# Kernel optimization log

Hardware: AMD Instinct MI355X
Metric: run time of the kernel (lower is better)

The kernel has to match this reference:

```python
import jax, jax.numpy as jnp
import numpy as np

N = 100000   # full-order dimension (mesh nodes)
n = 10       # reduced basis size
M_CLUSTERS = 8
K = 16       # neighbors per node
B = 4        # batch
MU = 20.0


def setup_inputs() -> dict:
    key = jax.random.key(0)
    k1, k2, k3, k4, k5, k6, k7 = jax.random.split(key, 7)
    x = jax.random.normal(k1, (B, N), dtype=jnp.float32)
    # torch.nn.Linear default init scale ~ 1/sqrt(fan_in)
    W_enc = jax.random.normal(k2, (n, N), dtype=jnp.float32) / np.sqrt(N)
    W_dec = jax.random.normal(k3, (n, N), dtype=jnp.float32) / np.sqrt(N)
    W_bw = jax.random.normal(k4, (n * M_CLUSTERS, n), dtype=jnp.float32) / np.sqrt(n)
    # small neighbor distances so every bubble window has a positive entry
    neighbour_distance = jax.random.uniform(k5, (N, K), dtype=jnp.float32) * 0.05
    neighbour_id = jax.random.randint(k6, (N, K), 0, N)
    clustering_labels = jax.random.randint(k7, (N,), 0, M_CLUSTERS)
    return {"x": x, "W_enc": W_enc, "W_dec": W_dec, "W_bw": W_bw,
            "neighbour_distance": neighbour_distance,
            "neighbour_id": neighbour_id,
            "clustering_labels": clustering_labels}


def reference(x, W_enc, W_dec, W_bw, neighbour_distance, neighbour_id, clustering_labels):
    # encode: Linear(N, n, bias=False)
    enc = x @ W_enc.T                                   # [B, n]
    # bandwidths: sigmoid + affine into [4/(60*mu), 1/60]
    bw = jax.nn.sigmoid(enc @ W_bw.T)                   # [B, n*m]
    lo = 4.0 / 60.0 / MU
    bw = (1.0 / 60.0 - lo) * bw + lo
    bw = bw.reshape(-1, n, M_CLUSTERS)                  # [B, n, m]
    bw = bw[:, :, clustering_labels]                    # [B, n, N] per-node bandwidth
    # bubble window over neighbors (vectorized over all groups at once;
    # group loop in the original writes disjoint node slices -> identical math)
    d2 = neighbour_distance ** 2                        # [N, K]
    denom = (bw * MU) ** 2                              # [B, n, N]
    window = jax.nn.relu(1.0 - d2[None, None] / denom[..., None])  # [B, n, N, K]
    window = window / jnp.sum(window, axis=-1, keepdims=True)
    # gather neighbor basis values: decoder.weight[:, neighbour_id]
    basis_nb = W_dec[:, neighbour_id]                   # [n, N, K]
    smoothed = jnp.einsum('cNk,bcNk->bcN', basis_nb, window)  # [B, n, N]
    # decode: enc [B,1,n] bmm smoothed [B,n,N] -> [B,N]
    return jnp.einsum('bc,bcN->bN', enc, smoothed)
```

## Files before the change

### kernel.cpp

```cpp
#include <hip/hip_runtime.h>
#include <math.h>

#define NN 100000
#define NF 10
#define MC 8
#define KK 16
#define BB 4
#define MUF 20.0f

#define ENC_SLICES 32
#define ENC_BLOCKS (BB * NF * ENC_SLICES)
#define TR_BLOCKS  ((NN + 255) / 256)

__device__ __forceinline__ float frcp(float x) {
#if __has_builtin(__builtin_amdgcn_rcpf)
    return __builtin_amdgcn_rcpf(x);
#else
    return 1.0f / x;
#endif
}

template <bool TR>
__global__ __launch_bounds__(256) void k_prep(const float* __restrict__ x,
                                              const float* __restrict__ Wenc,
                                              const float* __restrict__ Wdec,
                                              float* __restrict__ part,
                                              float* __restrict__ Wt) {
    int blk = blockIdx.x;
    if (blk < ENC_BLOCKS) {
        int pair  = blk >> 5;
        int slice = blk & 31;
        int b = pair / NF, c = pair % NF;
        const int chunk = NN / ENC_SLICES;
        int j0 = slice * chunk;
        int j1 = j0 + chunk;
        const float* xp = x + (size_t)b * NN;
        const float* wp = Wenc + (size_t)c * NN;
        float acc = 0.f;
        for (int j = j0 + threadIdx.x; j < j1; j += 256)
            acc = fmaf(xp[j], wp[j], acc);
#pragma unroll
        for (int off = 32; off; off >>= 1) acc += __shfl_down(acc, off);
        __shared__ float red[4];
        if ((threadIdx.x & 63) == 0) red[threadIdx.x >> 6] = acc;
        __syncthreads();
        if (threadIdx.x == 0) part[blk] = red[0] + red[1] + red[2] + red[3];
    } else if (TR) {
        int j = (blk - ENC_BLOCKS) * 256 + threadIdx.x;
        if (j < NN) {
            float tmp[16];
#pragma unroll
            for (int c = 0; c < NF; ++c) tmp[c] = Wdec[(size_t)c * NN + j];
#pragma unroll
            for (int c = NF; c < 16; ++c) tmp[c] = 0.f;
            float4* o = (float4*)(Wt + (size_t)j * 16);
            o[0] = make_float4(tmp[0], tmp[1], tmp[2], tmp[3]);
            o[1] = make_float4(tmp[4], tmp[5], tmp[6], tmp[7]);
            o[2] = make_float4(tmp[8], tmp[9], tmp[10], tmp[11]);
            o[3] = make_float4(tmp[12], tmp[13], tmp[14], tmp[15]);
        }
    }
}

template <bool TR>
__global__ __launch_bounds__(256) void k_main(const float* __restrict__ ndist,
                                              const int* __restrict__ nbid,
                                              const int* __restrict__ labels,
                                              const float* __restrict__ part,
                                              const float* __restrict__ Wbw,
                                              const float* __restrict__ Wsrc,
                                              float* __restrict__ out) {
    __shared__ float s_enc[BB * NF];
    __shared__ float s_dinv[BB * NF * MC];
    int tid = threadIdx.x;
    if (tid < BB * NF) {
        const float* p = part + tid * ENC_SLICES;
        float s = 0.f;
#pragma unroll
        for (int i = 0; i < ENC_SLICES; ++i) s += p[i];
        s_enc[tid] = s;
    }
    __syncthreads();
    for (int t = tid; t < BB * NF * MC; t += 256) {
        int b = t / (NF * MC);
        int r = t % (NF * MC);
        float z = 0.f;
#pragma unroll
        for (int c = 0; c < NF; ++c) z = fmaf(s_enc[b * NF + c], Wbw[r * NF + c], z);
        float sig = 1.f / (1.f + __expf(-z));
        const float lo = (float)(4.0 / 60.0 / 20.0);
        const float sc = (float)(1.0 / 60.0 - 4.0 / 60.0 / 20.0);
        float bwv = fmaf(sc, sig, lo) * MUF;
        s_dinv[t] = frcp(bwv * bwv);
    }
    __syncthreads();

    int g = blockIdx.x * 256 + tid;
    int j = g >> 1;
    if (j >= NN) return;
    int bh = (g & 1) << 1;

    int lab = labels[j];
    float dA[NF], dB[NF];
#pragma unroll
    for (int c = 0; c < NF; ++c) {
        dA[c] = s_dinv[(bh)     * (NF * MC) + c * MC + lab];
        dB[c] = s_dinv[(bh + 1) * (NF * MC) + c * MC + lab];
    }

    const float4* dp = (const float4*)(ndist + (size_t)j * KK);
    float4 q0 = dp[0], q1 = dp[1], q2 = dp[2], q3 = dp[3];
    const int4* np = (const int4*)(nbid + (size_t)j * KK);
    int4 i0 = np[0], i1 = np[1], i2 = np[2], i3 = np[3];
    float nd[KK] = {q0.x, q0.y, q0.z, q0.w, q1.x, q1.y, q1.z, q1.w,
                    q2.x, q2.y, q2.z, q2.w, q3.x, q3.y, q3.z, q3.w};
    int nb[KK] = {i0.x, i0.y, i0.z, i0.w, i1.x, i1.y, i1.z, i1.w,
                  i2.x, i2.y, i2.z, i2.w, i3.x, i3.y, i3.z, i3.w};

    float wsA[NF], smA[NF], wsB[NF], smB[NF];
#pragma unroll
    for (int c = 0; c < NF; ++c) { wsA[c] = 0.f; smA[c] = 0.f; wsB[c] = 0.f; smB[c] = 0.f; }

#pragma unroll
    for (int k = 0; k < KK; ++k) {
        float d = nd[k];
        float dd = d * d;
        float bas[12];
        if (TR) {
            const float4* bp = (const float4*)(Wsrc + (size_t)(unsigned)nb[k] * 16);
            float4 b0 = bp[0], b1 = bp[1], b2 = bp[2];
            bas[0] = b0.x; bas[1] = b0.y; bas[2] = b0.z; bas[3] = b0.w;
            bas[4] = b1.x; bas[5] = b1.y; bas[6] = b1.z; bas[7] = b1.w;
            bas[8] = b2.x; bas[9] = b2.y; bas[10] = b2.z; bas[11] = b2.w;
        } else {
#pragma unroll
            for (int c = 0; c < NF; ++c) bas[c] = Wsrc[(size_t)c * NN + nb[k]];
        }
#pragma unroll
        for (int c = 0; c < NF; ++c) {
            float wA = fmaxf(fmaf(-dd, dA[c], 1.f), 0.f);
            wsA[c] += wA; smA[c] = fmaf(wA, bas[c], smA[c]);
            float wB = fmaxf(fmaf(-dd, dB[c], 1.f), 0.f);
            wsB[c] += wB; smB[c] = fmaf(wB, bas[c], smB[c]);
        }
    }

    float accA = 0.f, accB = 0.f;
#pragma unroll
    for (int c = 0; c < NF; ++c) {
        accA = fmaf(s_enc[bh * NF + c],       smA[c] * frcp(wsA[c]), accA);
        accB = fmaf(s_enc[(bh + 1) * NF + c], smB[c] * frcp(wsB[c]), accB);
    }
    out[(size_t)bh * NN + j]       = accA;
    out[(size_t)(bh + 1) * NN + j] = accB;
}

extern "C" void kernel_launch(void* const* d_in, const int* in_sizes, int n_in,
                              void* d_out, int out_size, void* d_ws, size_t ws_size,
                              hipStream_t stream) {
    const float* x      = (const float*)d_in[0];
    const float* Wenc   = (const float*)d_in[1];
    const float* Wdec   = (const float*)d_in[2];
    const float* Wbw    = (const float*)d_in[3];
    const float* ndist  = (const float*)d_in[4];
    const int*   nbid   = (const int*)d_in[5];
    const int*   labels = (const int*)d_in[6];
    float* out = (float*)d_out;

    float* part = (float*)d_ws;
    float* Wt   = (float*)((char*)d_ws + 8192);
    size_t need = 8192 + (size_t)NN * 16 * sizeof(float);
    bool tr = (ws_size >= need);

    int main_blocks = (NN * 2 + 255) / 256;

    if (tr) {
        k_prep<true><<<ENC_BLOCKS + TR_BLOCKS, 256, 0, stream>>>(x, Wenc, Wdec, part, Wt);
        k_main<true><<<main_blocks, 256, 0, stream>>>(ndist, nbid, labels, part, Wbw, Wt, out);
    } else {
        k_prep<false><<<ENC_BLOCKS, 256, 0, stream>>>(x, Wenc, Wdec, part, nullptr);
        k_main<false><<<main_blocks, 256, 0, stream>>>(ndist, nbid, labels, part, Wbw, Wdec, out);
    }
}
```

Before: 112.7 us.

## Fuse encoder dot products across batch and split main work by feature

The encoder stage now has each block compute all 40 batch-feature dot products over one chunk of nodes, so x and W_enc are each read once instead of once per pair. Partial sums go through a two-level reduction at the start of the main kernel. The main kernel's two threads per node now split the features (4+1 each) and cover all four batches, then combine results with a lane shuffle. Each thread gathers 5 basis values per neighbour instead of 12, which lowers gather traffic per thread. The cost is a longer reduction prologue in every main block and more per-thread register state.

New measurement: 116.0 us. +2.9%, slower.

```diff
diff --git a/kernel.cpp b/kernel.cpp
--- a/kernel.cpp
+++ b/kernel.cpp
@@ -8,9 +8,9 @@
 #define BB 4
 #define MUF 20.0f
 
-#define ENC_SLICES 32
-#define ENC_BLOCKS (BB * NF * ENC_SLICES)
-#define TR_BLOCKS  ((NN + 255) / 256)
+#define PB  200
+#define JCH (NN / PB)
+#define TRB ((NN + 255) / 256)
 
 __device__ __forceinline__ float frcp(float x) {
 #if __has_builtin(__builtin_amdgcn_rcpf)
@@ -27,26 +27,43 @@
                                               float* __restrict__ part,
                                               float* __restrict__ Wt) {
     int blk = blockIdx.x;
-    if (blk < ENC_BLOCKS) {
-        int pair  = blk >> 5;
-        int slice = blk & 31;
-        int b = pair / NF, c = pair % NF;
-        const int chunk = NN / ENC_SLICES;
-        int j0 = slice * chunk;
-        int j1 = j0 + chunk;
-        const float* xp = x + (size_t)b * NN;
-        const float* wp = Wenc + (size_t)c * NN;
-        float acc = 0.f;
-        for (int j = j0 + threadIdx.x; j < j1; j += 256)
-            acc = fmaf(xp[j], wp[j], acc);
-#pragma unroll
-        for (int off = 32; off; off >>= 1) acc += __shfl_down(acc, off);
-        __shared__ float red[4];
-        if ((threadIdx.x & 63) == 0) red[threadIdx.x >> 6] = acc;
+    if (blk < PB) {
+        int j0 = blk * JCH;
+        float acc[BB * NF];
+#pragma unroll
+        for (int i = 0; i < BB * NF; ++i) acc[i] = 0.f;
+        for (int jj = threadIdx.x; jj < JCH; jj += 256) {
+            int j = j0 + jj;
+            float xv[BB], wv[NF];
+#pragma unroll
+            for (int b = 0; b < BB; ++b) xv[b] = x[(size_t)b * NN + j];
+#pragma unroll
+            for (int c = 0; c < NF; ++c) wv[c] = Wenc[(size_t)c * NN + j];
+#pragma unroll
+            for (int b = 0; b < BB; ++b)
+#pragma unroll
+                for (int c = 0; c < NF; ++c)
+                    acc[b * NF + c] = fmaf(xv[b], wv[c], acc[b * NF + c]);
+        }
+#pragma unroll
+        for (int i = 0; i < BB * NF; ++i) {
+            float v = acc[i];
+#pragma unroll
+            for (int off = 32; off; off >>= 1) v += __shfl_down(v, off, 64);
+            acc[i] = v;
+        }
+        __shared__ float red[BB * NF][4];
+        int lane = threadIdx.x & 63, w = threadIdx.x >> 6;
+        if (lane == 0) {
+#pragma unroll
+            for (int i = 0; i < BB * NF; ++i) red[i][w] = acc[i];
+        }
         __syncthreads();
-        if (threadIdx.x == 0) part[blk] = red[0] + red[1] + red[2] + red[3];
+        if (threadIdx.x < BB * NF)
+            part[threadIdx.x * PB + blk] =
+                red[threadIdx.x][0] + red[threadIdx.x][1] + red[threadIdx.x][2] + red[threadIdx.x][3];
     } else if (TR) {
-        int j = (blk - ENC_BLOCKS) * 256 + threadIdx.x;
+        int j = (blk - PB) * 256 + threadIdx.x;
         if (j < NN) {
             float tmp[16];
 #pragma unroll
@@ -72,12 +89,21 @@
                                               float* __restrict__ out) {
     __shared__ float s_enc[BB * NF];
     __shared__ float s_dinv[BB * NF * MC];
+    __shared__ float s_red[BB * NF][6];
     int tid = threadIdx.x;
+    if (tid < 240) {
+        int p = tid / 6, s = tid % 6;
+        int i0 = s * 34, i1 = i0 + 34 > PB ? PB : i0 + 34;
+        const float* pp = part + p * PB;
+        float sum = 0.f;
+        for (int i = i0; i < i1; ++i) sum += pp[i];
+        s_red[p][s] = sum;
+    }
+    __syncthreads();
     if (tid < BB * NF) {
-        const float* p = part + tid * ENC_SLICES;
         float s = 0.f;
 #pragma unroll
-        for (int i = 0; i < ENC_SLICES; ++i) s += p[i];
+        for (int i = 0; i < 6; ++i) s += s_red[tid][i];
         s_enc[tid] = s;
     }
     __syncthreads();
@@ -98,61 +124,77 @@
     int g = blockIdx.x * 256 + tid;
     int j = g >> 1;
     if (j >= NN) return;
-    int bh = (g & 1) << 1;
+    int cg = g & 1;
+    int cbase = cg * 4;
+    int cext  = 8 + cg;
 
     int lab = labels[j];
-    float dA[NF], dB[NF];
-#pragma unroll
-    for (int c = 0; c < NF; ++c) {
-        dA[c] = s_dinv[(bh)     * (NF * MC) + c * MC + lab];
-        dB[c] = s_dinv[(bh + 1) * (NF * MC) + c * MC + lab];
+    float dv[BB][5];
+#pragma unroll
+    for (int b = 0; b < BB; ++b) {
+#pragma unroll
+        for (int i = 0; i < 4; ++i)
+            dv[b][i] = s_dinv[b * (NF * MC) + (cbase + i) * MC + lab];
+        dv[b][4] = s_dinv[b * (NF * MC) + cext * MC + lab];
     }
 
     const float4* dp = (const float4*)(ndist + (size_t)j * KK);
     float4 q0 = dp[0], q1 = dp[1], q2 = dp[2], q3 = dp[3];
     const int4* np = (const int4*)(nbid + (size_t)j * KK);
-    int4 i0 = np[0], i1 = np[1], i2 = np[2], i3 = np[3];
+    int4 i0v = np[0], i1v = np[1], i2v = np[2], i3v = np[3];
     float nd[KK] = {q0.x, q0.y, q0.z, q0.w, q1.x, q1.y, q1.z, q1.w,
                     q2.x, q2.y, q2.z, q2.w, q3.x, q3.y, q3.z, q3.w};
-    int nb[KK] = {i0.x, i0.y, i0.z, i0.w, i1.x, i1.y, i1.z, i1.w,
-                  i2.x, i2.y, i2.z, i2.w, i3.x, i3.y, i3.z, i3.w};
-
-    float wsA[NF], smA[NF], wsB[NF], smB[NF];
-#pragma unroll
-    for (int c = 0; c < NF; ++c) { wsA[c] = 0.f; smA[c] = 0.f; wsB[c] = 0.f; smB[c] = 0.f; }
+    int nb[KK] = {i0v.x, i0v.y, i0v.z, i0v.w, i1v.x, i1v.y, i1v.z, i1v.w,
+                  i2v.x, i2v.y, i2v.z, i2v.w, i3v.x, i3v.y, i3v.z, i3v.w};
+
+    float ws[BB][5], sm[BB][5];
+#pragma unroll
+    for (int b = 0; b < BB; ++b)
+#pragma unroll
+        for (int i = 0; i < 5; ++i) { ws[b][i] = 0.f; sm[b][i] = 0.f; }
 
 #pragma unroll
     for (int k = 0; k < KK; ++k) {
         float d = nd[k];
         float dd = d * d;
-        float bas[12];
+        float bas[5];
         if (TR) {
-            const float4* bp = (const float4*)(Wsrc + (size_t)(unsigned)nb[k] * 16);
-            float4 b0 = bp[0], b1 = bp[1], b2 = bp[2];
-            bas[0] = b0.x; bas[1] = b0.y; bas[2] = b0.z; bas[3] = b0.w;
-            bas[4] = b1.x; bas[5] = b1.y; bas[6] = b1.z; bas[7] = b1.w;
-            bas[8] = b2.x; bas[9] = b2.y; bas[10] = b2.z; bas[11] = b2.w;
+            const float* row = Wsrc + (size_t)(unsigned)nb[k] * 16;
+            float4 bq = ((const float4*)row)[cg];
+            float be = row[cext];
+            bas[0] = bq.x; bas[1] = bq.y; bas[2] = bq.z; bas[3] = bq.w; bas[4] = be;
         } else {
 #pragma unroll
-            for (int c = 0; c < NF; ++c) bas[c] = Wsrc[(size_t)c * NN + nb[k]];
-        }
-#pragma unroll
-        for (int c = 0; c < NF; ++c) {
-            float wA = fmaxf(fmaf(-dd, dA[c], 1.f), 0.f);
-            wsA[c] += wA; smA[c] = fmaf(wA, bas[c], smA[c]);
-            float wB = fmaxf(fmaf(-dd, dB[c], 1.f), 0.f);
-            wsB[c] += wB; smB[c] = fmaf(wB, bas[c], smB[c]);
-        }
-    }
-
-    float accA = 0.f, accB = 0.f;
-#pragma unroll
-    for (int c = 0; c < NF; ++c) {
-        accA = fmaf(s_enc[bh * NF + c],       smA[c] * frcp(wsA[c]), accA);
-        accB = fmaf(s_enc[(bh + 1) * NF + c], smB[c] * frcp(wsB[c]), accB);
-    }
-    out[(size_t)bh * NN + j]       = accA;
-    out[(size_t)(bh + 1) * NN + j] = accB;
+            for (int i = 0; i < 4; ++i)
+                bas[i] = Wsrc[(size_t)(cbase + i) * NN + (unsigned)nb[k]];
+            bas[4] = Wsrc[(size_t)cext * NN + (unsigned)nb[k]];
+        }
+#pragma unroll
+        for (int i = 0; i < 5; ++i)
+#pragma unroll
+            for (int b = 0; b < BB; ++b) {
+                float w = fmaxf(fmaf(-dd, dv[b][i], 1.f), 0.f);
+                ws[b][i] += w;
+                sm[b][i] = fmaf(w, bas[i], sm[b][i]);
+            }
+    }
+
+    float pbv[BB];
+#pragma unroll
+    for (int b = 0; b < BB; ++b) {
+        float acc = 0.f;
+#pragma unroll
+        for (int i = 0; i < 4; ++i)
+            acc = fmaf(s_enc[b * NF + cbase + i], sm[b][i] * frcp(ws[b][i]), acc);
+        acc = fmaf(s_enc[b * NF + cext], sm[b][4] * frcp(ws[b][4]), acc);
+        pbv[b] = acc;
+    }
+#pragma unroll
+    for (int b = 0; b < BB; ++b) pbv[b] += __shfl_xor(pbv[b], 1, 64);
+    if (cg == 0) {
+#pragma unroll
+        for (int b = 0; b < BB; ++b) out[(size_t)b * NN + j] = pbv[b];
+    }
 }
 
 extern "C" void kernel_launch(void* const* d_in, const int* in_sizes, int n_in,
@@ -168,17 +210,17 @@
     float* out = (float*)d_out;
 
     float* part = (float*)d_ws;
-    float* Wt   = (float*)((char*)d_ws + 8192);
-    size_t need = 8192 + (size_t)NN * 16 * sizeof(float);
+    float* Wt   = (float*)((char*)d_ws + 32768);
+    size_t need = 32768 + (size_t)NN * 16 * sizeof(float);
     bool tr = (ws_size >= need);
 
     int main_blocks = (NN * 2 + 255) / 256;
 
     if (tr) {
-        k_prep<true><<<ENC_BLOCKS + TR_BLOCKS, 256, 0, stream>>>(x, Wenc, Wdec, part, Wt);
+        k_prep<true><<<PB + TRB, 256, 0, stream>>>(x, Wenc, Wdec, part, Wt);
         k_main<true><<<main_blocks, 256, 0, stream>>>(ndist, nbid, labels, part, Wbw, Wt, out);
     } else {
-        k_prep<false><<<ENC_BLOCKS, 256, 0, stream>>>(x, Wenc, Wdec, part, nullptr);
+        k_prep<false><<<PB, 256, 0, stream>>>(x, Wenc, Wdec, part, nullptr);
         k_main<false><<<main_blocks, 256, 0, stream>>>(ndist, nbid, labels, part, Wbw, Wdec, out);
     }
 }
```

## Fuse prep and main kernels into one cooperative launch with grid sync

Applied to the files above, without the earlier changes.

Merges the encoder-reduction/transpose kernel and the bubble-smoothing kernel into a single cooperative kernel of 782 blocks separated by a grid-wide barrier. The encoder reduction now uses 9 slices per (batch, basis) pair instead of 32, so the encoder blocks and the transpose blocks fit together within the main grid. The goal is to drop the second launch and the inter-kernel gap. In exchange it relies on cooperative launch support and all blocks being co-resident (launch bounds 256,4), and falls back to two launches on failure. Fewer slices means each encoder block does a longer serial reduction.

Result: slower. 240.1 us (+113.0%).

```diff
diff --git a/kernel.cpp b/kernel.cpp
--- a/kernel.cpp
+++ b/kernel.cpp
@@ -1,5 +1,8 @@
 #include <hip/hip_runtime.h>
+#include <hip/hip_cooperative_groups.h>
 #include <math.h>
+
+namespace cg = cooperative_groups;
 
 #define NN 100000
 #define NF 10
@@ -8,9 +11,11 @@
 #define BB 4
 #define MUF 20.0f
 
-#define ENC_SLICES 32
-#define ENC_BLOCKS (BB * NF * ENC_SLICES)
-#define TR_BLOCKS  ((NN + 255) / 256)
+#define GRID 782
+#define TRB  391
+#define ESL  9
+#define EB   (BB * NF * ESL)
+#define ECH  ((NN + ESL - 1) / ESL)
 
 __device__ __forceinline__ float frcp(float x) {
 #if __has_builtin(__builtin_amdgcn_rcpf)
@@ -21,63 +26,64 @@
 }
 
 template <bool TR>
-__global__ __launch_bounds__(256) void k_prep(const float* __restrict__ x,
-                                              const float* __restrict__ Wenc,
-                                              const float* __restrict__ Wdec,
-                                              float* __restrict__ part,
-                                              float* __restrict__ Wt) {
-    int blk = blockIdx.x;
-    if (blk < ENC_BLOCKS) {
-        int pair  = blk >> 5;
-        int slice = blk & 31;
+__device__ __forceinline__ void phaseA(const float* __restrict__ x,
+                                       const float* __restrict__ Wenc,
+                                       const float* __restrict__ Wdec,
+                                       float* __restrict__ part,
+                                       float* __restrict__ Wt,
+                                       int blk, int tid) {
+    if (blk < TRB) {
+        if (TR) {
+            int j = blk * 256 + tid;
+            if (j < NN) {
+                float tmp[16];
+#pragma unroll
+                for (int c = 0; c < NF; ++c) tmp[c] = Wdec[(size_t)c * NN + j];
+#pragma unroll
+                for (int c = NF; c < 16; ++c) tmp[c] = 0.f;
+                float4* o = (float4*)(Wt + (size_t)j * 16);
+                o[0] = make_float4(tmp[0], tmp[1], tmp[2], tmp[3]);
+                o[1] = make_float4(tmp[4], tmp[5], tmp[6], tmp[7]);
+                o[2] = make_float4(tmp[8], tmp[9], tmp[10], tmp[11]);
+                o[3] = make_float4(tmp[12], tmp[13], tmp[14], tmp[15]);
+            }
+        }
+    } else if (blk < TRB + EB) {
+        int eblk = blk - TRB;
+        int pair = eblk / ESL, slice = eblk % ESL;
         int b = pair / NF, c = pair % NF;
-        const int chunk = NN / ENC_SLICES;
-        int j0 = slice * chunk;
-        int j1 = j0 + chunk;
+        int j0 = slice * ECH;
+        int j1 = j0 + ECH; if (j1 > NN) j1 = NN;
         const float* xp = x + (size_t)b * NN;
         const float* wp = Wenc + (size_t)c * NN;
         float acc = 0.f;
-        for (int j = j0 + threadIdx.x; j < j1; j += 256)
+        for (int j = j0 + tid; j < j1; j += 256)
             acc = fmaf(xp[j], wp[j], acc);
 #pragma unroll
-        for (int off = 32; off; off >>= 1) acc += __shfl_down(acc, off);
+        for (int off = 32; off; off >>= 1) acc += __shfl_down(acc, off, 64);
         __shared__ float red[4];
-        if ((threadIdx.x & 63) == 0) red[threadIdx.x >> 6] = acc;
+        if ((tid & 63) == 0) red[tid >> 6] = acc;
         __syncthreads();
-        if (threadIdx.x == 0) part[blk] = red[0] + red[1] + red[2] + red[3];
-    } else if (TR) {
-        int j = (blk - ENC_BLOCKS) * 256 + threadIdx.x;
-        if (j < NN) {
-            float tmp[16];
-#pragma unroll
-            for (int c = 0; c < NF; ++c) tmp[c] = Wdec[(size_t)c * NN + j];
-#pragma unroll
-            for (int c = NF; c < 16; ++c) tmp[c] = 0.f;
-            float4* o = (float4*)(Wt + (size_t)j * 16);
-            o[0] = make_float4(tmp[0], tmp[1], tmp[2], tmp[3]);
-            o[1] = make_float4(tmp[4], tmp[5], tmp[6], tmp[7]);
-            o[2] = make_float4(tmp[8], tmp[9], tmp[10], tmp[11]);
-            o[3] = make_float4(tmp[12], tmp[13], tmp[14], tmp[15]);
-        }
-    }
-}
-
-template <bool TR>
-__global__ __launch_bounds__(256) void k_main(const float* __restrict__ ndist,
-                                              const int* __restrict__ nbid,
-                                              const int* __restrict__ labels,
-                                              const float* __restrict__ part,
-                                              const float* __restrict__ Wbw,
-                                              const float* __restrict__ Wsrc,
-                                              float* __restrict__ out) {
+        if (tid == 0) part[eblk] = red[0] + red[1] + red[2] + red[3];
+    }
+}
+
+template <bool TR>
+__device__ __forceinline__ void phaseB(const float* __restrict__ ndist,
+                                       const int* __restrict__ nbid,
+                                       const int* __restrict__ labels,
+                                       const float* __restrict__ part,
+                                       const float* __restrict__ Wbw,
+                                       const float* __restrict__ Wsrc,
+                                       float* __restrict__ out,
+                                       int blk, int tid) {
     __shared__ float s_enc[BB * NF];
     __shared__ float s_dinv[BB * NF * MC];
-    int tid = threadIdx.x;
     if (tid < BB * NF) {
-        const float* p = part + tid * ENC_SLICES;
+        const float* p = part + tid * ESL;
         float s = 0.f;
 #pragma unroll
-        for (int i = 0; i < ENC_SLICES; ++i) s += p[i];
+        for (int i = 0; i < ESL; ++i) s += p[i];
         s_enc[tid] = s;
     }
     __syncthreads();
@@ -95,90 +101,124 @@
     }
     __syncthreads();
 
-    int g = blockIdx.x * 256 + tid;
+    int g = blk * 256 + tid;
     int j = g >> 1;
     if (j >= NN) return;
     int bh = (g & 1) << 1;
 
     int lab = labels[j];
-    float dA[NF], dB[NF];
-#pragma unroll
-    for (int c = 0; c < NF; ++c) {
-        dA[c] = s_dinv[(bh)     * (NF * MC) + c * MC + lab];
-        dB[c] = s_dinv[(bh + 1) * (NF * MC) + c * MC + lab];
-    }
+    float dv[2][NF];
+#pragma unroll
+    for (int b2 = 0; b2 < 2; ++b2)
+#pragma unroll
+        for (int c = 0; c < NF; ++c)
+            dv[b2][c] = s_dinv[(bh + b2) * (NF * MC) + c * MC + lab];
+
+    float ws[2][NF], sm[2][NF];
+#pragma unroll
+    for (int b2 = 0; b2 < 2; ++b2)
+#pragma unroll
+        for (int c = 0; c < NF; ++c) { ws[b2][c] = 0.f; sm[b2][c] = 0.f; }
 
     const float4* dp = (const float4*)(ndist + (size_t)j * KK);
-    float4 q0 = dp[0], q1 = dp[1], q2 = dp[2], q3 = dp[3];
-    const int4* np = (const int4*)(nbid + (size_t)j * KK);
-    int4 i0 = np[0], i1 = np[1], i2 = np[2], i3 = np[3];
-    float nd[KK] = {q0.x, q0.y, q0.z, q0.w, q1.x, q1.y, q1.z, q1.w,
-                    q2.x, q2.y, q2.z, q2.w, q3.x, q3.y, q3.z, q3.w};
-    int nb[KK] = {i0.x, i0.y, i0.z, i0.w, i1.x, i1.y, i1.z, i1.w,
-                  i2.x, i2.y, i2.z, i2.w, i3.x, i3.y, i3.z, i3.w};
-
-    float wsA[NF], smA[NF], wsB[NF], smB[NF];
-#pragma unroll
-    for (int c = 0; c < NF; ++c) { wsA[c] = 0.f; smA[c] = 0.f; wsB[c] = 0.f; smB[c] = 0.f; }
-
-#pragma unroll
-    for (int k = 0; k < KK; ++k) {
-        float d = nd[k];
-        float dd = d * d;
-        float bas[12];
-        if (TR) {
-            const float4* bp = (const float4*)(Wsrc + (size_t)(unsigned)nb[k] * 16);
-            float4 b0 = bp[0], b1 = bp[1], b2 = bp[2];
-            bas[0] = b0.x; bas[1] = b0.y; bas[2] = b0.z; bas[3] = b0.w;
-            bas[4] = b1.x; bas[5] = b1.y; bas[6] = b1.z; bas[7] = b1.w;
-            bas[8] = b2.x; bas[9] = b2.y; bas[10] = b2.z; bas[11] = b2.w;
-        } else {
-#pragma unroll
-            for (int c = 0; c < NF; ++c) bas[c] = Wsrc[(size_t)c * NN + nb[k]];
+    const int4*   np = (const int4*)(nbid + (size_t)j * KK);
+
+#pragma unroll
+    for (int q = 0; q < 4; ++q) {
+        float4 d4 = dp[q];
+        int4   n4 = np[q];
+        float dd4[4] = {d4.x * d4.x, d4.y * d4.y, d4.z * d4.z, d4.w * d4.w};
+        int    id4[4] = {n4.x, n4.y, n4.z, n4.w};
+#pragma unroll
+        for (int kk = 0; kk < 4; ++kk) {
+            float dd = dd4[kk];
+            float bas[12];
+            if (TR) {
+                const float4* bp = (const float4*)(Wsrc + (size_t)(unsigned)id4[kk] * 16);
+                float4 b0 = bp[0], b1 = bp[1], b2 = bp[2];
+                bas[0] = b0.x; bas[1] = b0.y; bas[2] = b0.z; bas[3] = b0.w;
+                bas[4] = b1.x; bas[5] = b1.y; bas[6] = b1.z; bas[7] = b1.w;
+                bas[8] = b2.x; bas[9] = b2.y; bas[10] = b2.z; bas[11] = b2.w;
+            } else {
+#pragma unroll
+                for (int c = 0; c < NF; ++c)
+                    bas[c] = Wsrc[(size_t)c * NN + (unsigned)id4[kk]];
+            }
+#pragma unroll
+            for (int c = 0; c < NF; ++c)
+#pragma unroll
+                for (int b2 = 0; b2 < 2; ++b2) {
+                    float w = fmaxf(fmaf(-dd, dv[b2][c], 1.f), 0.f);
+                    ws[b2][c] += w;
+                    sm[b2][c] = fmaf(w, bas[c], sm[b2][c]);
+                }
         }
-#pragma unroll
-        for (int c = 0; c < NF; ++c) {
-            float wA = fmaxf(fmaf(-dd, dA[c], 1.f), 0.f);
-            wsA[c] += wA; smA[c] = fmaf(wA, bas[c], smA[c]);
-            float wB = fmaxf(fmaf(-dd, dB[c], 1.f), 0.f);
-            wsB[c] += wB; smB[c] = fmaf(wB, bas[c], smB[c]);
-        }
-    }
-
-    float accA = 0.f, accB = 0.f;
-#pragma unroll
-    for (int c = 0; c < NF; ++c) {
-        accA = fmaf(s_enc[bh * NF + c],       smA[c] * frcp(wsA[c]), accA);
-        accB = fmaf(s_enc[(bh + 1) * NF + c], smB[c] * frcp(wsB[c]), accB);
-    }
-    out[(size_t)bh * NN + j]       = accA;
-    out[(size_t)(bh + 1) * NN + j] = accB;
+    }
+
+#pragma unroll
+    for (int b2 = 0; b2 < 2; ++b2) {
+        float acc = 0.f;
+#pragma unroll
+        for (int c = 0; c < NF; ++c)
+            acc = fmaf(s_enc[(bh + b2) * NF + c], sm[b2][c] * frcp(ws[b2][c]), acc);
+        out[(size_t)(bh + b2) * NN + j] = acc;
+    }
+}
+
+template <bool TR>
+__global__ __launch_bounds__(256, 4) void k_fused(const float* ndist, const int* nbid,
+                                                  const int* labels, const float* x,
+                                                  const float* Wenc, const float* Wdec,
+                                                  const float* Wbw, float* part,
+                                                  float* Wt, float* out) {
+    phaseA<TR>(x, Wenc, Wdec, part, Wt, blockIdx.x, threadIdx.x);
+    cg::this_grid().sync();
+    phaseB<TR>(ndist, nbid, labels, part, Wbw, TR ? Wt : Wdec, out,
+               blockIdx.x, threadIdx.x);
+}
+
+template <bool TR>
+__global__ __launch_bounds__(256) void k_A(const float* x, const float* Wenc,
+                                           const float* Wdec, float* part, float* Wt) {
+    phaseA<TR>(x, Wenc, Wdec, part, Wt, blockIdx.x, threadIdx.x);
+}
+
+template <bool TR>
+__global__ __launch_bounds__(256) void k_B(const float* ndist, const int* nbid,
+                                           const int* labels, const float* part,
+                                           const float* Wbw, const float* Wsrc,
+                                           float* out) {
+    phaseB<TR>(ndist, nbid, labels, part, Wbw, Wsrc, out, blockIdx.x, threadIdx.x);
 }
 
 extern "C" void kernel_launch(void* const* d_in, const int* in_sizes, int n_in,
                               void* d_out, int out_size, void* d_ws, size_t ws_size,
                               hipStream_t stream) {
+    const float* ndist  = (const float*)d_in[4];
+    const int*   nbid   = (const int*)d_in[5];
+    const int*   labels = (const int*)d_in[6];
     const float* x      = (const float*)d_in[0];
     const float* Wenc   = (const float*)d_in[1];
     const float* Wdec   = (const float*)d_in[2];
     const float* Wbw    = (const float*)d_in[3];
-    const float* ndist  = (const float*)d_in[4];
-    const int*   nbid   = (const int*)d_in[5];
-    const int*   labels = (const int*)d_in[6];
-    float* out = (float*)d_out;
-
+    float* out  = (float*)d_out;
     float* part = (float*)d_ws;
-    float* Wt   = (float*)((char*)d_ws + 8192);
-    size_t need = 8192 + (size_t)NN * 16 * sizeof(float);
-    bool tr = (ws_size >= need);
-
-    int main_blocks = (NN * 2 + 255) / 256;
-
-    if (tr) {
-        k_prep<true><<<ENC_BLOCKS + TR_BLOCKS, 256, 0, stream>>>(x, Wenc, Wdec, part, Wt);
-        k_main<true><<<main_blocks, 256, 0, stream>>>(ndist, nbid, labels, part, Wbw, Wt, out);
+    float* Wt   = (float*)((char*)d_ws + 32768);
+    size_t need = 32768 + (size_t)NN * 16 * sizeof(float);
+
+    if (ws_size >= need) {
+        void* args[] = {(void*)&ndist, (void*)&nbid, (void*)&labels, (void*)&x,
+                        (void*)&Wenc, (void*)&Wdec, (void*)&Wbw, (void*)&part,
+                        (void*)&Wt, (void*)&out};
+        hipError_t e = hipLaunchCooperativeKernel(
+            reinterpret_cast<const void*>(&k_fused<true>),
+            dim3(GRID), dim3(256), args, 0u, stream);
+        if (e != hipSuccess) {
+            k_A<true><<<GRID, 256, 0, stream>>>(x, Wenc, Wdec, part, Wt);
+            k_B<true><<<GRID, 256, 0, stream>>>(ndist, nbid, labels, part, Wbw, Wt, out);
+        }
     } else {
-        k_prep<false><<<ENC_BLOCKS, 256, 0, stream>>>(x, Wenc, Wdec, part, nullptr);
-        k_main<false><<<main_blocks, 256, 0, stream>>>(ndist, nbid, labels, part, Wbw, Wdec, out);
-    }
-}
+        k_A<false><<<GRID, 256, 0, stream>>>(x, Wenc, Wdec, part, nullptr);
+        k_B<false><<<GRID, 256, 0, stream>>>(ndist, nbid, labels, part, Wbw, Wdec, out);
+    }
+}
```
